# Performance work log

Measured on AMD Instinct MI355X. Metric: run time of the kernel, lower is better.

Reference implementation:

```python
import jax, jax.numpy as jnp
import numpy as np

B, S, D, H = 2, 2048, 1024, 16
AD = D // H  # per-head dim = 64


def setup_inputs() -> dict:
    key = jax.random.key(0)
    k1, k2, k3 = jax.random.split(key, 3)
    x = jax.random.normal(k1, (B, S, D), dtype=jnp.float32)
    W_qkv = jax.random.normal(k2, (D, 3 * D), dtype=jnp.float32) * (1.0 / np.sqrt(D))
    b_qkv = jax.random.normal(k3, (3 * D,), dtype=jnp.float32) * 0.01
    return {"x": x, "W_qkv": W_qkv, "b_qkv": b_qkv}


def reference(x, W_qkv, b_qkv):
    b, s, _ = x.shape
    qkv = x @ W_qkv + b_qkv                      # [B,S,3D]
    qkv = qkv.reshape(b, s, H, 3 * AD)           # per-head interleaved qkv
    qkv = jnp.transpose(qkv, (0, 2, 1, 3))       # [B,H,S,3*ad]
    q = qkv[..., :AD]
    k = qkv[..., AD:2 * AD]
    v = qkv[..., 2 * AD:]
    scale = 1.0 / jnp.sqrt(jnp.asarray(AD, dtype=x.dtype))
    att = jnp.einsum("bhqd,bhkd->bhqk", q, k) * scale  # [B,H,S,S]
    att = jax.nn.softmax(att, axis=-1)
    values = jnp.einsum("bhqk,bhkd->bhqd", att, v)     # [B,H,S,ad]
    # Faithful to source: reshape [B,H,S,ad] -> [B,S,ad*H] WITHOUT head transpose
    return values.reshape(b, s, AD * H)
```

## Files before the change

### kernel.cpp

```cpp
#include <hip/hip_runtime.h>
#include <stdint.h>
#include <stddef.h>

#define S_LEN 2048
#define NH 16
#define HD 64
#define DM 1024
#define NQKV 3072
#define MROWS 4096
#define NBH 32

typedef float f32x4 __attribute__((ext_vector_type(4)));
typedef float f32x16 __attribute__((ext_vector_type(16)));
typedef __bf16 bf16x8 __attribute__((ext_vector_type(8)));
typedef __bf16 bf16x4 __attribute__((ext_vector_type(4)));
typedef __bf16 bf16x2v __attribute__((ext_vector_type(2)));
typedef short short8_t __attribute__((ext_vector_type(8)));
typedef unsigned int u32x4 __attribute__((ext_vector_type(4)));

__device__ __forceinline__ unsigned short f2bf(float f) {
  union { float f; unsigned int u; } v; v.f = f;
  unsigned int u = v.u;
  u += 0x7FFFu + ((u >> 16) & 1u);
  return (unsigned short)(u >> 16);
}

__device__ __forceinline__ void async_copy16(const void* g, void* l) {
  __builtin_amdgcn_global_load_lds(
      (const __attribute__((address_space(1))) void*)g,
      (__attribute__((address_space(3))) void*)l, 16, 0, 0);
}

#define WAITCNT_BARRIER(N)                                          \
  asm volatile("s_waitcnt vmcnt(" #N ")" ::: "memory");             \
  __builtin_amdgcn_sched_barrier(0);                                \
  __builtin_amdgcn_s_barrier();                                     \
  __builtin_amdgcn_sched_barrier(0);

__global__ __launch_bounds__(256) void cast_x_kernel(const float* __restrict__ x,
                                                     unsigned short* __restrict__ xb) {
  size_t i = ((size_t)blockIdx.x * 256 + threadIdx.x) * 8;
  f32x4 a = *(const f32x4*)(x + i);
  f32x4 b = *(const f32x4*)(x + i + 4);
  union { unsigned short u[8]; short8_t v; } o;
  o.u[0] = f2bf(a[0]); o.u[1] = f2bf(a[1]); o.u[2] = f2bf(a[2]); o.u[3] = f2bf(a[3]);
  o.u[4] = f2bf(b[0]); o.u[5] = f2bf(b[1]); o.u[6] = f2bf(b[2]); o.u[7] = f2bf(b[3]);
  *(short8_t*)(xb + i) = o.v;
}

__global__ __launch_bounds__(256) void transpose_w_kernel(const float* __restrict__ W,
                                                          unsigned short* __restrict__ wt) {
  __shared__ float tile[32][33];
  const int n0 = blockIdx.x * 32;
  const int k0 = blockIdx.y * 32;
  const int tx = threadIdx.x;
  const int ty = threadIdx.y;
  #pragma unroll
  for (int i = 0; i < 4; ++i)
    tile[ty + i * 8][tx] = W[(size_t)(k0 + ty + i * 8) * NQKV + n0 + tx];
  __syncthreads();
  #pragma unroll
  for (int i = 0; i < 4; ++i)
    wt[(size_t)(n0 + ty + i * 8) * DM + k0 + tx] = f2bf(tile[tx][ty + i * 8]);
}

__global__ __launch_bounds__(256) void qkv_gemm_kernel(
    const unsigned short* __restrict__ xb, const unsigned short* __restrict__ wt,
    const float* __restrict__ bias,
    unsigned short* __restrict__ Qb, unsigned short* __restrict__ Kb,
    unsigned short* __restrict__ Vt) {
  __shared__ __align__(16) unsigned char Sh[4][128 * 64 * 2];
  const int t = threadIdx.x;
  const int lane = t & 63;
  const int wave = t >> 6;
  const int wm = (wave >> 1) * 64, wn = (wave & 1) * 64;
  const int lr = lane & 15, g = lane >> 4;
  const int m0 = blockIdx.x * 128, n0 = blockIdx.y * 128;

  f32x4 acc[4][4];
  #pragma unroll
  for (int i = 0; i < 4; ++i)
    #pragma unroll
    for (int j = 0; j < 4; ++j) acc[i][j] = f32x4{0.f, 0.f, 0.f, 0.f};

  auto stage = [&](int kt, int buf) __attribute__((always_inline)) {
    const int k0 = kt * 64;
    #pragma unroll
    for (int i = 0; i < 4; ++i) {
      int c = t + i * 256;
      int row = c >> 3;
      int cc = (c & 7) ^ (row & 7);
      async_copy16(xb + (size_t)(m0 + row) * DM + k0 + cc * 8, Sh[buf * 2] + c * 16);
      async_copy16(wt + (size_t)(n0 + row) * DM + k0 + cc * 8, Sh[buf * 2 + 1] + c * 16);
    }
  };

  auto compute = [&](int buf) __attribute__((always_inline)) {
    unsigned char* const As = Sh[buf * 2];
    unsigned char* const Bs = Sh[buf * 2 + 1];
    bf16x8 af[2][4], bfr[2][4];
    #pragma unroll
    for (int kk = 0; kk < 2; ++kk) {
      #pragma unroll
      for (int i = 0; i < 4; ++i) {
        int ra = wm + i * 16 + lr;
        af[kk][i] = *(const bf16x8*)(As + ((ra * 128 + kk * 64 + g * 16) ^ ((ra & 7) << 4)));
        int rb = wn + i * 16 + lr;
        bfr[kk][i] = *(const bf16x8*)(Bs + ((rb * 128 + kk * 64 + g * 16) ^ ((rb & 7) << 4)));
      }
    }
    __builtin_amdgcn_s_setprio(1);
    #pragma unroll
    for (int kk = 0; kk < 2; ++kk)
      #pragma unroll
      for (int mi = 0; mi < 4; ++mi)
        #pragma unroll
        for (int ni = 0; ni < 4; ++ni)
          acc[mi][ni] = __builtin_amdgcn_mfma_f32_16x16x32_bf16(
              af[kk][mi], bfr[kk][ni], acc[mi][ni], 0, 0, 0);
    __builtin_amdgcn_s_setprio(0);
  };

  stage(0, 0);
  __syncthreads();
  for (int kt = 0; kt < DM / 64; kt += 2) {
    stage(kt + 1, 1);
    compute(0);
    __syncthreads();
    if (kt + 2 < DM / 64) stage(kt + 2, 0);
    compute(1);
    __syncthreads();
  }

  const float QSC = 0.18033688011112042f;
  const int nbase = n0 + wn;
  const int h = nbase / 192;
  const int typ = (nbase % 192) >> 6;
  const int b = m0 >> 11;
  const int bh = b * NH + h;

  if (typ == 2) {
    unsigned char* const T = Sh[0] + wave * 8192;
    #pragma unroll
    for (int ni = 0; ni < 4; ++ni) {
      int col = ni * 16 + lr;
      float bv = bias[nbase + col];
      #pragma unroll
      for (int mi = 0; mi < 4; ++mi) {
        bf16x4 w;
        w[0] = (__bf16)(acc[mi][ni][0] + bv);
        w[1] = (__bf16)(acc[mi][ni][1] + bv);
        w[2] = (__bf16)(acc[mi][ni][2] + bv);
        w[3] = (__bf16)(acc[mi][ni][3] + bv);
        int byte = (col * 128 + (mi * 16 + g * 4) * 2) ^ ((col & 7) << 4);
        *(bf16x4*)(T + byte) = w;
      }
    }
    asm volatile("s_waitcnt lgkmcnt(0)" ::: "memory");
    __builtin_amdgcn_sched_barrier(0);
    const int s0 = (m0 & 2047) + wm + (lane & 7) * 8;
    #pragma unroll
    for (int i = 0; i < 8; ++i) {
      int col = i * 8 + (lane >> 3);
      int byte = (col * 128 + (lane & 7) * 16) ^ ((col & 7) << 4);
      bf16x8 v = *(const bf16x8*)(T + byte);
      *(bf16x8*)(Vt + ((size_t)bh * HD + col) * S_LEN + s0) = v;
    }
  } else {
    unsigned short* const dst = (typ == 0) ? Qb : Kb;
    const float sc = (typ == 0) ? QSC : 1.0f;
    #pragma unroll
    for (int ni = 0; ni < 4; ++ni) {
      int d = ni * 16 + lr;
      float bv = bias[nbase + d];
      #pragma unroll
      for (int mi = 0; mi < 4; ++mi) {
        #pragma unroll
        for (int r = 0; r < 4; ++r) {
          int s = (m0 & 2047) + wm + mi * 16 + g * 4 + r;
          dst[((size_t)bh * S_LEN + s) * HD + d] = f2bf((acc[mi][ni][r] + bv) * sc);
        }
      }
    }
  }
}

__global__ __launch_bounds__(256) void attn_kernel(
    const unsigned short* __restrict__ Qb, const unsigned short* __restrict__ Kb,
    const unsigned short* __restrict__ Vt, float* __restrict__ out) {
  __shared__ __align__(16) unsigned char smem[49152];
  const int t = threadIdx.x;
  const int lane = t & 63;
  const int wave = t >> 6;
  const int l5 = lane & 31, hi = lane >> 5;
  const int bh = blockIdx.y;
  const int q0 = blockIdx.x * 128 + wave * 32;

  const unsigned short* Kbh = Kb + (size_t)bh * S_LEN * HD;
  const unsigned short* Vbh = Vt + (size_t)bh * HD * S_LEN;

  const unsigned short* Qrow = Qb + ((size_t)bh * S_LEN + q0 + l5) * HD;
  bf16x8 qf[4];
  #pragma unroll
  for (int ks = 0; ks < 4; ++ks)
    qf[ks] = *(const bf16x8*)(Qrow + ks * 16 + hi * 8);

  union { unsigned short u[8]; bf16x8 v; } one_c;
  #pragma unroll
  for (int j = 0; j < 8; ++j) one_c.u[j] = 0x3F80;
  const bf16x8 ones8 = one_c.v;

  int kvOff[2][4];
  #pragma unroll
  for (int rb = 0; rb < 2; ++rb)
    #pragma unroll
    for (int ks = 0; ks < 4; ++ks) {
      int r = rb * 32 + l5;
      kvOff[rb][ks] = (r * 128 + ks * 32 + hi * 16) ^ ((l5 & 7) << 4);
    }

  const int c0 = t, c1 = t + 256;
  const int row0 = c0 >> 3, row1 = c1 >> 3;
  const int cc0 = (c0 & 7) ^ (row0 & 7), cc1 = (c1 & 7) ^ (row1 & 7);
  const int kGO0 = row0 * HD + cc0 * 8, kGO1 = row1 * HD + cc1 * 8;
  const int vGO0 = row0 * S_LEN + cc0 * 8, vGO1 = row1 * S_LEN + cc1 * 8;

  f32x16 oacc0, oacc1, lacc;
  #pragma unroll
  for (int i = 0; i < 16; ++i) { oacc0[i] = 0.f; oacc1[i] = 0.f; lacc[i] = 0.f; }

  auto stage = [&](int kt, int buf) __attribute__((always_inline)) {
    const unsigned short* kp = Kbh + (size_t)kt * (64 * HD);
    const unsigned short* vp = Vbh + kt * 64;
    unsigned char* const base = smem + buf * 16384;
    async_copy16(kp + kGO0, base + c0 * 16);
    async_copy16(kp + kGO1, base + c1 * 16);
    async_copy16(vp + vGO0, base + 8192 + c0 * 16);
    async_copy16(vp + vGO1, base + 8192 + c1 * 16);
  };

  auto compute = [&](int buf) __attribute__((always_inline)) {
    unsigned char* const Ksb = smem + buf * 16384;
    unsigned char* const Vsb = Ksb + 8192;

    f32x16 sacc0, sacc1;
    #pragma unroll
    for (int i = 0; i < 16; ++i) { sacc0[i] = 0.f; sacc1[i] = 0.f; }
    __builtin_amdgcn_s_setprio(1);
    #pragma unroll
    for (int ks = 0; ks < 4; ++ks) {
      bf16x8 kf0 = *(const bf16x8*)(Ksb + kvOff[0][ks]);
      sacc0 = __builtin_amdgcn_mfma_f32_32x32x16_bf16(kf0, qf[ks], sacc0, 0, 0, 0);
      bf16x8 kf1 = *(const bf16x8*)(Ksb + kvOff[1][ks]);
      sacc1 = __builtin_amdgcn_mfma_f32_32x32x16_bf16(kf1, qf[ks], sacc1, 0, 0, 0);
    }
    __builtin_amdgcn_s_setprio(0);

    unsigned wv0[8], wv1[8];
    #pragma unroll
    for (int rr = 0; rr < 8; ++rr) {
      bf16x2v ca;
      ca[0] = (__bf16)exp2f(sacc0[2 * rr]);
      ca[1] = (__bf16)exp2f(sacc0[2 * rr + 1]);
      wv0[rr] = __builtin_bit_cast(unsigned, ca);
      bf16x2v cb;
      cb[0] = (__bf16)exp2f(sacc1[2 * rr]);
      cb[1] = (__bf16)exp2f(sacc1[2 * rr + 1]);
      wv1[rr] = __builtin_bit_cast(unsigned, cb);
    }

    __builtin_amdgcn_s_setprio(1);
    #pragma unroll
    for (int kstep = 0; kstep < 4; ++kstep) {
      const int kkl = kstep & 1;
      unsigned a0, a1, b0, b1;
      if (kstep < 2) { a0 = wv0[4 * kkl]; a1 = wv0[4 * kkl + 1]; b0 = wv0[4 * kkl + 2]; b1 = wv0[4 * kkl + 3]; }
      else           { a0 = wv1[4 * kkl]; a1 = wv1[4 * kkl + 1]; b0 = wv1[4 * kkl + 2]; b1 = wv1[4 * kkl + 3]; }
      asm("v_permlane32_swap_b32 %0, %1" : "+v"(a0), "+v"(b0));
      asm("v_permlane32_swap_b32 %0, %1" : "+v"(a1), "+v"(b1));
      u32x4 tmp; tmp[0] = a0; tmp[1] = a1; tmp[2] = b0; tmp[3] = b1;
      bf16x8 pf = __builtin_bit_cast(bf16x8, tmp);
      bf16x8 vf0 = *(const bf16x8*)(Vsb + kvOff[0][kstep]);
      oacc0 = __builtin_amdgcn_mfma_f32_32x32x16_bf16(vf0, pf, oacc0, 0, 0, 0);
      bf16x8 vf1 = *(const bf16x8*)(Vsb + kvOff[1][kstep]);
      oacc1 = __builtin_amdgcn_mfma_f32_32x32x16_bf16(vf1, pf, oacc1, 0, 0, 0);
      lacc = __builtin_amdgcn_mfma_f32_32x32x16_bf16(ones8, pf, lacc, 0, 0, 0);
    }
    __builtin_amdgcn_s_setprio(0);
  };

  stage(0, 0);
  stage(1, 1);
  for (int kt3 = 0; kt3 < 30; kt3 += 3) {
    WAITCNT_BARRIER(4); stage(kt3 + 2, 2); compute(0);
    WAITCNT_BARRIER(4); stage(kt3 + 3, 0); compute(1);
    WAITCNT_BARRIER(4); stage(kt3 + 4, 1); compute(2);
  }
  WAITCNT_BARRIER(4); compute(0);
  WAITCNT_BARRIER(0); compute(1);

  float inv = 1.0f / lacc[0];
  float* outp = out + ((size_t)bh * S_LEN + q0 + l5) * HD;
  #pragma unroll
  for (int b = 0; b < 4; ++b) {
    f32x4 o0, o1;
    #pragma unroll
    for (int j = 0; j < 4; ++j) {
      o0[j] = oacc0[b * 4 + j] * inv;
      o1[j] = oacc1[b * 4 + j] * inv;
    }
    *(f32x4*)(outp + b * 8 + hi * 4) = o0;
    *(f32x4*)(outp + 32 + b * 8 + hi * 4) = o1;
  }
}

extern "C" void kernel_launch(void* const* d_in, const int* in_sizes, int n_in,
                              void* d_out, int out_size, void* d_ws, size_t ws_size,
                              hipStream_t stream) {
  const float* x    = (const float*)d_in[0];
  const float* W    = (const float*)d_in[1];
  const float* bias = (const float*)d_in[2];
  float* out = (float*)d_out;

  unsigned short* xb = (unsigned short*)d_ws;
  unsigned short* wt = xb + (size_t)MROWS * DM;
  unsigned short* Qb = wt + (size_t)NQKV * DM;
  unsigned short* Kb = Qb + (size_t)NBH * S_LEN * HD;
  unsigned short* Vt = Kb + (size_t)NBH * S_LEN * HD;

  cast_x_kernel<<<(MROWS * DM) / (256 * 8), 256, 0, stream>>>(x, xb);
  transpose_w_kernel<<<dim3(NQKV / 32, DM / 32), dim3(32, 8), 0, stream>>>(W, wt);
  qkv_gemm_kernel<<<dim3(MROWS / 128, NQKV / 128), 256, 0, stream>>>(xb, wt, bias, Qb, Kb, Vt);
  attn_kernel<<<dim3(S_LEN / 128, NBH), 256, 0, stream>>>(Qb, Kb, Vt, out);
}
```

Measured before the change: 100.3 us.

## Software-pipeline QK^T of next tile with softmax-PV of current tile

Splits the per-tile attention compute into a QK^T stage and an exp/PV stage. The loop now runs QK^T for tile k+1 before softmax and PV for tile k, so MFMA work can overlap the exp2 VALU work. The K/V ring buffer grows from three to four stages (64KB LDS) to keep an extra tile resident. This costs more registers for two sets of score accumulators and more LDS, which may reduce occupancy.

```diff
diff --git a/kernel.cpp b/kernel.cpp
--- a/kernel.cpp
+++ b/kernel.cpp
@@ -188,7 +188,7 @@
 __global__ __launch_bounds__(256) void attn_kernel(
     const unsigned short* __restrict__ Qb, const unsigned short* __restrict__ Kb,
     const unsigned short* __restrict__ Vt, float* __restrict__ out) {
-  __shared__ __align__(16) unsigned char smem[49152];
+  __shared__ __align__(16) unsigned char smem[65536];
   const int t = threadIdx.x;
   const int lane = t & 63;
   const int wave = t >> 6;
@@ -239,36 +239,35 @@
     async_copy16(vp + vGO1, base + 8192 + c1 * 16);
   };
 
-  auto compute = [&](int buf) __attribute__((always_inline)) {
+  auto qk = [&](int buf, f32x16& s0, f32x16& s1) __attribute__((always_inline)) {
     unsigned char* const Ksb = smem + buf * 16384;
-    unsigned char* const Vsb = Ksb + 8192;
-
-    f32x16 sacc0, sacc1;
-    #pragma unroll
-    for (int i = 0; i < 16; ++i) { sacc0[i] = 0.f; sacc1[i] = 0.f; }
+    #pragma unroll
+    for (int i = 0; i < 16; ++i) { s0[i] = 0.f; s1[i] = 0.f; }
     __builtin_amdgcn_s_setprio(1);
     #pragma unroll
     for (int ks = 0; ks < 4; ++ks) {
       bf16x8 kf0 = *(const bf16x8*)(Ksb + kvOff[0][ks]);
-      sacc0 = __builtin_amdgcn_mfma_f32_32x32x16_bf16(kf0, qf[ks], sacc0, 0, 0, 0);
+      s0 = __builtin_amdgcn_mfma_f32_32x32x16_bf16(kf0, qf[ks], s0, 0, 0, 0);
       bf16x8 kf1 = *(const bf16x8*)(Ksb + kvOff[1][ks]);
-      sacc1 = __builtin_amdgcn_mfma_f32_32x32x16_bf16(kf1, qf[ks], sacc1, 0, 0, 0);
+      s1 = __builtin_amdgcn_mfma_f32_32x32x16_bf16(kf1, qf[ks], s1, 0, 0, 0);
     }
     __builtin_amdgcn_s_setprio(0);
-
+  };
+
+  auto smpv = [&](int buf, f32x16& s0, f32x16& s1) __attribute__((always_inline)) {
+    unsigned char* const Vsb = smem + buf * 16384 + 8192;
     unsigned wv0[8], wv1[8];
     #pragma unroll
     for (int rr = 0; rr < 8; ++rr) {
       bf16x2v ca;
-      ca[0] = (__bf16)exp2f(sacc0[2 * rr]);
-      ca[1] = (__bf16)exp2f(sacc0[2 * rr + 1]);
+      ca[0] = (__bf16)exp2f(s0[2 * rr]);
+      ca[1] = (__bf16)exp2f(s0[2 * rr + 1]);
       wv0[rr] = __builtin_bit_cast(unsigned, ca);
       bf16x2v cb;
-      cb[0] = (__bf16)exp2f(sacc1[2 * rr]);
-      cb[1] = (__bf16)exp2f(sacc1[2 * rr + 1]);
+      cb[0] = (__bf16)exp2f(s1[2 * rr]);
+      cb[1] = (__bf16)exp2f(s1[2 * rr + 1]);
       wv1[rr] = __builtin_bit_cast(unsigned, cb);
     }
-
     __builtin_amdgcn_s_setprio(1);
     #pragma unroll
     for (int kstep = 0; kstep < 4; ++kstep) {
@@ -289,15 +288,23 @@
     __builtin_amdgcn_s_setprio(0);
   };
 
-  stage(0, 0);
-  stage(1, 1);
-  for (int kt3 = 0; kt3 < 30; kt3 += 3) {
-    WAITCNT_BARRIER(4); stage(kt3 + 2, 2); compute(0);
-    WAITCNT_BARRIER(4); stage(kt3 + 3, 0); compute(1);
-    WAITCNT_BARRIER(4); stage(kt3 + 4, 1); compute(2);
+  f32x16 sA0, sA1, sB0, sB1;
+
+  stage(0, 0); stage(1, 1); stage(2, 2);
+  WAITCNT_BARRIER(8);
+  qk(0, sA0, sA1);
+
+  for (int tt = 0; tt < 7; ++tt) {
+    const int tb = tt * 4;
+    WAITCNT_BARRIER(4); stage(tb + 3, 3); qk(1, sB0, sB1); smpv(0, sA0, sA1);
+    WAITCNT_BARRIER(4); stage(tb + 4, 0); qk(2, sA0, sA1); smpv(1, sB0, sB1);
+    WAITCNT_BARRIER(4); stage(tb + 5, 1); qk(3, sB0, sB1); smpv(2, sA0, sA1);
+    WAITCNT_BARRIER(4); stage(tb + 6, 2); qk(0, sA0, sA1); smpv(3, sB0, sB1);
   }
-  WAITCNT_BARRIER(4); compute(0);
-  WAITCNT_BARRIER(0); compute(1);
+  WAITCNT_BARRIER(4); stage(31, 3); qk(1, sB0, sB1); smpv(0, sA0, sA1);
+  WAITCNT_BARRIER(4);               qk(2, sA0, sA1); smpv(1, sB0, sB1);
+  WAITCNT_BARRIER(0);               qk(3, sB0, sB1); smpv(2, sA0, sA1);
+                                                     smpv(3, sB0, sB1);
 
   float inv = 1.0f / lacc[0];
   float* outp = out + ((size_t)bh * S_LEN + q0 + l5) * HD;
```

Result: no change. 99.81 us (-0.4%).
